# Performance work log

Measured on AMD Instinct MI355X. Metric: run time of the kernel, lower is better.

Reference implementation:

```python
import jax, jax.numpy as jnp
import numpy as np

B, N, T, L, H = 8, 128, 256, 32, 128


def setup_inputs() -> dict:
    key = jax.random.key(0)
    k0, k1, k2, k3, k4, k5 = jax.random.split(key, 6)
    x = jax.random.uniform(k0, (B, N, T), dtype=jnp.float32)
    s = 1.0 / np.sqrt(H)  # pytorch LSTM/Linear default init scale
    W_ih = jax.random.uniform(k1, (N, 4 * H, L), minval=-s, maxval=s, dtype=jnp.float32)
    b_ih = jax.random.uniform(k2, (N, 4 * H), minval=-s, maxval=s, dtype=jnp.float32)
    b_hh = jax.random.uniform(k3, (N, 4 * H), minval=-s, maxval=s, dtype=jnp.float32)
    W_fc = jax.random.uniform(k4, (N, N, H), minval=-s, maxval=s, dtype=jnp.float32)  # [node_i, out_j, H]
    b_fc = jax.random.uniform(k5, (N, N), minval=-s, maxval=s, dtype=jnp.float32)  # [node_i, out_j]
    return {"x": x, "W_ih": W_ih, "b_ih": b_ih, "b_hh": b_hh, "W_fc": W_fc, "b_fc": b_fc}


def reference(x, W_ih, b_ih, b_hh, W_fc, b_fc):
    # x: [B, N, T]
    Bn, Nn, Tn = x.shape
    Ln = W_ih.shape[-1]
    Hh = W_fc.shape[-1]
    Ttau = Tn - Ln  # number of prediction steps (t = L .. T-1)

    # Sliding windows x[:, i, tau:tau+L] for tau = 0..Ttau-1  -> [B, N, Ttau, L]
    idx = jnp.arange(Ttau)[:, None] + jnp.arange(Ln)[None, :]  # [Ttau, L]
    xw = x[:, :, idx]

    # Single-step LSTM with zero initial state: W_hh term vanishes.
    gates = jnp.einsum('bntl,ngl->bntg', xw, W_ih) + (b_ih + b_hh)[None, :, None, :]
    gi, gf, gg, go = jnp.split(gates, 4, axis=-1)  # pytorch order: i, f, g, o
    c = jax.nn.sigmoid(gi) * jnp.tanh(gg)          # f*c0 = 0
    h = jax.nn.sigmoid(go) * jnp.tanh(c)           # [B, N, Ttau, H]

    # Per-node fc (grouped GEMM): contributions[b, tau, j, i]
    contrib = jnp.einsum('bnth,njh->btjn', h, W_fc) + b_fc.T[None, None, :, :]

    # G[b, j, i] = mean_tau contrib[b, tau, j, i] / x[b, i, L + tau]
    denom = jnp.transpose(x[:, :, Ln:], (0, 2, 1))[:, :, None, :]  # [B, Ttau, 1, N_i]
    G = jnp.mean(contrib / denom, axis=1)                          # [B, N, N]

    X_hat = jnp.sum(contrib, axis=2) + 1e-6  # [B, Ttau, N]
    return G, X_hat
```

## Files before the change

kernel.cpp:

```cpp
#include <hip/hip_runtime.h>
#include <math.h>

#define B_  8
#define N_  128
#define T_  256
#define L_  32
#define H_  128
#define TT_ 224

typedef float f4    __attribute__((ext_vector_type(4)));
typedef float f32x4 __attribute__((ext_vector_type(4)));
typedef short bf16x8 __attribute__((ext_vector_type(8)));

__device__ __forceinline__ float fsig(float x) {
    return __builtin_amdgcn_rcpf(1.0f + __expf(-x));
}
__device__ __forceinline__ float ftanh_(float x) {
    return 1.0f - 2.0f * __builtin_amdgcn_rcpf(1.0f + __expf(2.0f * x));
}
__device__ __forceinline__ unsigned pk2bf(float a, float b) {
    unsigned ua = __float_as_uint(a), ub = __float_as_uint(b);
    ua = (ua + 0x7FFFu + ((ua >> 16) & 1u)) >> 16;
    ub = (ub + 0x7FFFu + ((ub >> 16) & 1u)) >> 16;
    return ua | (ub << 16);
}

__global__ __launch_bounds__(256)
void k_pre(const float* __restrict__ W_ih, const float* __restrict__ W_fc,
           const float* __restrict__ b_ih, const float* __restrict__ b_hh,
           const float* __restrict__ b_fc,
           unsigned short* __restrict__ W3sw, float* __restrict__ wsum,
           float* __restrict__ bsum, float* __restrict__ bia_g) {
    const int n   = blockIdx.x;
    const int pid = blockIdx.y;
    const int tid = threadIdx.x;
    if (pid < 6) {
        const int idx  = pid * 256 + tid;
        const int fg   = idx >> 6;
        const int lane = idx & 63;
        const int col  = lane & 15, quad = lane >> 4;
        const int g    = fg % 3, ht = fg / 3;
        const int r    = g * 128 + ht * 16 + col;
        const int sr   = r + (r >= 128 ? 128 : 0);
        const f4* src = (const f4*)(W_ih + (size_t)n * 512 * L_ + sr * L_ + quad * 8);
        f4 v0 = src[0], v1 = src[1];
        uint4 out;
        out.x = pk2bf(v0.x, v0.y); out.y = pk2bf(v0.z, v0.w);
        out.z = pk2bf(v1.x, v1.y); out.w = pk2bf(v1.z, v1.w);
        *(uint4*)&W3sw[((size_t)n * 1536 + idx) * 8] = out;
    } else {
        __shared__ f4 part[8][32];
        __shared__ float bp[2];
        {
            const int h4 = tid & 31, jg = tid >> 5;
            const f4* Wf = (const f4*)(W_fc + (size_t)n * N_ * H_) + (size_t)jg * 16 * 32 + h4;
            f4 s = {0.f, 0.f, 0.f, 0.f};
            #pragma unroll
            for (int j = 0; j < 16; ++j) s += Wf[j * 32];
            part[jg][h4] = s;
        }
        if (tid < 128) {
            float bv = b_fc[n * N_ + tid];
            #pragma unroll
            for (int off = 32; off > 0; off >>= 1) bv += __shfl_down(bv, off, 64);
            if ((tid & 63) == 0) bp[tid >> 6] = bv;
        }
        for (int i = tid; i < 384; i += 256) {
            const int sr = i + (i >= 128 ? 128 : 0);
            bia_g[n * 384 + i] = b_ih[(size_t)n * 512 + sr] + b_hh[(size_t)n * 512 + sr];
        }
        __syncthreads();
        if (tid < 32) {
            f4 s = part[0][tid];
            #pragma unroll
            for (int jg = 1; jg < 8; ++jg) s += part[jg][tid];
            *(f4*)&wsum[n * H_ + tid * 4] = s;
        }
        if (tid == 0) bsum[n] = bp[0] + bp[1];
    }
}

__global__ __launch_bounds__(256)
__attribute__((amdgpu_waves_per_eu(4, 4)))
void k_main(const float* __restrict__ x,
            const unsigned short* __restrict__ W3sw,
            const float* __restrict__ bia_g,
            const float* __restrict__ wsum, const float* __restrict__ bsum,
            const float* __restrict__ W_fc, const float* __restrict__ b_fc,
            float* __restrict__ G, float* __restrict__ xhat) {
    const int n   = blockIdx.x;
    const int b   = blockIdx.y;
    const int tid = threadIdx.x;
    const int w    = tid >> 6;
    const int lane = tid & 63;
    const int col  = lane & 15;
    const int quad = lane >> 4;

    __shared__ float xs[258];
    __shared__ unsigned xeo[2][128];
    __shared__ float xr[TT_];
    __shared__ float xh_part[4][TT_];
    __shared__ float hd_loc[H_];
    __shared__ float red[4];

    const uint4* wsw = (const uint4*)W3sw + (size_t)n * 24 * 64 + lane;
    union { uint4 u; bf16x8 v; } bfr[2][3];
    float biaL[2][3], wshL[2];
    #pragma unroll
    for (int ht2 = 0; ht2 < 2; ++ht2) {
        const int ht = 2 * w + ht2;
        #pragma unroll
        for (int g = 0; g < 3; ++g) {
            bfr[ht2][g].u = wsw[(size_t)(ht * 3 + g) * 64];
            biaL[ht2][g]  = bia_g[n * 384 + g * 128 + ht * 16 + col];
        }
        wshL[ht2] = wsum[n * H_ + ht * 16 + col];
    }
    const float bsum_n = bsum[n];

    xs[tid] = x[((size_t)b * N_ + n) * T_ + tid];
    if (tid < 2) xs[256 + tid] = 0.f;
    __syncthreads();
    if (tid < TT_) xr[tid] = 1.0f / xs[L_ + tid];
    if (tid < 128) {
        xeo[0][tid] = pk2bf(xs[2 * tid],     xs[2 * tid + 1]);
        xeo[1][tid] = pk2bf(xs[2 * tid + 1], xs[2 * tid + 2]);
    }
    __syncthreads();

    float hd_acc[2] = {0.f, 0.f};
    const f32x4 zero4 = {0.f, 0.f, 0.f, 0.f};

    for (int ttile = 0; ttile < 14; ++ttile) {
        const int s = ttile * 16 + col + quad * 8;
        const int p = s & 1, base = s >> 1;
        union { unsigned u[4]; bf16x8 v; } af;
        #pragma unroll
        for (int q = 0; q < 4; ++q) af.u[q] = xeo[p][base + q];

        const f4 xr4 = *(const f4*)&xr[ttile * 16 + quad * 4];
        float px[4] = {0.f, 0.f, 0.f, 0.f};

        #pragma unroll
        for (int ht2 = 0; ht2 < 2; ++ht2) {
            f32x4 ai = __builtin_amdgcn_mfma_f32_16x16x32_bf16(af.v, bfr[ht2][0].v, zero4, 0, 0, 0);
            f32x4 ag = __builtin_amdgcn_mfma_f32_16x16x32_bf16(af.v, bfr[ht2][1].v, zero4, 0, 0, 0);
            f32x4 ao = __builtin_amdgcn_mfma_f32_16x16x32_bf16(af.v, bfr[ht2][2].v, zero4, 0, 0, 0);
            #pragma unroll
            for (int reg = 0; reg < 4; ++reg) {
                const float gi = ai[reg] + biaL[ht2][0];
                const float gg = ag[reg] + biaL[ht2][1];
                const float go = ao[reg] + biaL[ht2][2];
                const float c  = fsig(gi) * ftanh_(gg);
                const float hh = fsig(go) * ftanh_(c);
                hd_acc[ht2] = fmaf(hh, xr4[reg], hd_acc[ht2]);
                px[reg]     = fmaf(hh, wshL[ht2], px[reg]);
            }
        }
        #pragma unroll
        for (int reg = 0; reg < 4; ++reg) {
            float pv = px[reg];
            pv += __shfl_xor(pv, 1, 64);
            pv += __shfl_xor(pv, 2, 64);
            pv += __shfl_xor(pv, 4, 64);
            pv += __shfl_xor(pv, 8, 64);
            if (col == 0) xh_part[w][ttile * 16 + quad * 4 + reg] = pv;
        }
    }

    #pragma unroll
    for (int ht2 = 0; ht2 < 2; ++ht2) {
        float v = hd_acc[ht2];
        v += __shfl_xor(v, 16, 64);
        v += __shfl_xor(v, 32, 64);
        if (lane < 16) hd_loc[(2 * w + ht2) * 16 + lane] = v;
    }
    {
        float dv = (tid < TT_) ? xr[tid] : 0.f;
        #pragma unroll
        for (int off = 32; off > 0; off >>= 1) dv += __shfl_down(dv, off, 64);
        if (lane == 0) red[w] = dv;
    }
    __syncthreads();

    if (tid < TT_) {
        const float v = xh_part[0][tid] + xh_part[1][tid] +
                        xh_part[2][tid] + xh_part[3][tid];
        xhat[((size_t)b * TT_ + tid) * N_ + n] = v + bsum_n + 1e-6f;
    }

    {
        const float dinv = red[0] + red[1] + red[2] + red[3];
        const int j    = tid >> 1;
        const int half = tid & 1;
        const f4* Wf = (const f4*)(W_fc + ((size_t)n * N_ + j) * H_ + half * 64);
        float s = 0.f;
        #pragma unroll
        for (int q = 0; q < 16; ++q) {
            const f4 wv = Wf[q];
            const int hb = half * 64 + q * 4;
            s = fmaf(wv.x, hd_loc[hb + 0],
                fmaf(wv.y, hd_loc[hb + 1],
                fmaf(wv.z, hd_loc[hb + 2],
                fmaf(wv.w, hd_loc[hb + 3], s))));
        }
        s += __shfl_xor(s, 1, 64);
        if (half == 0) {
            const float bj = b_fc[n * N_ + j];
            G[(size_t)b * N_ * N_ + (size_t)j * N_ + n] =
                (s + bj * dinv) * (1.0f / 224.0f);
        }
    }
}

extern "C" void kernel_launch(void* const* d_in, const int* in_sizes, int n_in,
                              void* d_out, int out_size, void* d_ws, size_t ws_size,
                              hipStream_t stream) {
    const float* x    = (const float*)d_in[0];
    const float* W_ih = (const float*)d_in[1];
    const float* b_ih = (const float*)d_in[2];
    const float* b_hh = (const float*)d_in[3];
    const float* W_fc = (const float*)d_in[4];
    const float* b_fc = (const float*)d_in[5];

    float* G    = (float*)d_out;
    float* xhat = (float*)d_out + (size_t)B_ * N_ * N_;

    unsigned short* W3sw = (unsigned short*)d_ws;
    float* wsum  = (float*)(W3sw + (size_t)N_ * 1536 * 8);
    float* bsum  = wsum + N_ * H_;
    float* bia_g = bsum + N_;

    k_pre<<<dim3(N_, 7), dim3(256), 0, stream>>>(W_ih, W_fc, b_ih, b_hh, b_fc,
                                                 W3sw, wsum, bsum, bia_g);
    k_main<<<dim3(N_, B_), dim3(256), 0, stream>>>(x, W3sw, bia_g, wsum, bsum,
                                                   W_fc, b_fc, G, xhat);
}
```

Baseline: 117.4 us.

## Merge sigmoid-tanh reciprocals and replace shuffle reduction with LDS atomics

Each sigmoid·tanh product is rewritten as a single ratio, (e2-1)/((1+e1)(e2+1)), so each gate pair needs one reciprocal instead of two. The per-tile butterfly shuffle reduction of the x_hat partials is replaced by LDS float atomicAdd into a padded [224][20] buffer, which is zeroed up front and summed with vector loads at the end. The t-tile loop is also unrolled by 2. This trades shuffle latency for LDS atomic traffic and adds about 18 KB of shared memory, which may affect occupancy. The merged formula can overflow to inf/inf for large gate values.

```diff
diff --git a/kernel.cpp b/kernel.cpp
--- a/kernel.cpp
+++ b/kernel.cpp
@@ -12,12 +12,6 @@
 typedef float f32x4 __attribute__((ext_vector_type(4)));
 typedef short bf16x8 __attribute__((ext_vector_type(8)));
 
-__device__ __forceinline__ float fsig(float x) {
-    return __builtin_amdgcn_rcpf(1.0f + __expf(-x));
-}
-__device__ __forceinline__ float ftanh_(float x) {
-    return 1.0f - 2.0f * __builtin_amdgcn_rcpf(1.0f + __expf(2.0f * x));
-}
 __device__ __forceinline__ unsigned pk2bf(float a, float b) {
     unsigned ua = __float_as_uint(a), ub = __float_as_uint(b);
     ua = (ua + 0x7FFFu + ((ua >> 16) & 1u)) >> 16;
@@ -99,7 +93,7 @@
     __shared__ float xs[258];
     __shared__ unsigned xeo[2][128];
     __shared__ float xr[TT_];
-    __shared__ float xh_part[4][TT_];
+    __shared__ float xh_acc[TT_ * 20];
     __shared__ float hd_loc[H_];
     __shared__ float red[4];
 
@@ -120,6 +114,7 @@
 
     xs[tid] = x[((size_t)b * N_ + n) * T_ + tid];
     if (tid < 2) xs[256 + tid] = 0.f;
+    for (int i = tid; i < TT_ * 20; i += 256) xh_acc[i] = 0.f;
     __syncthreads();
     if (tid < TT_) xr[tid] = 1.0f / xs[L_ + tid];
     if (tid < 128) {
@@ -131,6 +126,7 @@
     float hd_acc[2] = {0.f, 0.f};
     const f32x4 zero4 = {0.f, 0.f, 0.f, 0.f};
 
+    #pragma unroll 2
     for (int ttile = 0; ttile < 14; ++ttile) {
         const int s = ttile * 16 + col + quad * 8;
         const int p = s & 1, base = s >> 1;
@@ -151,21 +147,21 @@
                 const float gi = ai[reg] + biaL[ht2][0];
                 const float gg = ag[reg] + biaL[ht2][1];
                 const float go = ao[reg] + biaL[ht2][2];
-                const float c  = fsig(gi) * ftanh_(gg);
-                const float hh = fsig(go) * ftanh_(c);
+                const float e1 = __expf(-gi);
+                const float e2 = __expf(gg + gg);
+                const float c  = (e2 - 1.f) *
+                    __builtin_amdgcn_rcpf((1.f + e1) * (e2 + 1.f));
+                const float e3 = __expf(-go);
+                const float e4 = __expf(c + c);
+                const float hh = (e4 - 1.f) *
+                    __builtin_amdgcn_rcpf((1.f + e3) * (e4 + 1.f));
                 hd_acc[ht2] = fmaf(hh, xr4[reg], hd_acc[ht2]);
                 px[reg]     = fmaf(hh, wshL[ht2], px[reg]);
             }
         }
         #pragma unroll
-        for (int reg = 0; reg < 4; ++reg) {
-            float pv = px[reg];
-            pv += __shfl_xor(pv, 1, 64);
-            pv += __shfl_xor(pv, 2, 64);
-            pv += __shfl_xor(pv, 4, 64);
-            pv += __shfl_xor(pv, 8, 64);
-            if (col == 0) xh_part[w][ttile * 16 + quad * 4 + reg] = pv;
-        }
+        for (int reg = 0; reg < 4; ++reg)
+            atomicAdd(&xh_acc[(ttile * 16 + quad * 4 + reg) * 20 + col], px[reg]);
     }
 
     #pragma unroll
@@ -184,9 +180,11 @@
     __syncthreads();
 
     if (tid < TT_) {
-        const float v = xh_part[0][tid] + xh_part[1][tid] +
-                        xh_part[2][tid] + xh_part[3][tid];
-        xhat[((size_t)b * TT_ + tid) * N_ + n] = v + bsum_n + 1e-6f;
+        const float* row = &xh_acc[tid * 20];
+        const f4 a = *(const f4*)row + *(const f4*)(row + 4) +
+                     *(const f4*)(row + 8) + *(const f4*)(row + 12);
+        xhat[((size_t)b * TT_ + tid) * N_ + n] =
+            (a[0] + a[1] + a[2] + a[3]) + bsum_n + 1e-6f;
     }
 
     {
```

After: 163.2 us. 39.0% more time.
